# Kernel tuning notes

Hardware: AMD Instinct MI355X
Metric: run time of the kernel (lower is better)

Reference implementation:

```python
import jax, jax.numpy as jnp
import numpy as np

N_NODES = 50000
N_EDGES = 800000
NUM_FEATURES = 256
HIDDEN = 128
NUM_CLASSES = 64


def gcn_conv(x, edge_index, W, b):
    """PyG-style GCNConv: out = D^-1/2 (A+I) D^-1/2 (x W) + b.

    edge_index[0] = source (j), edge_index[1] = target (i);
    messages flow source -> target and are summed at the target.
    """
    n = x.shape[0]
    loop = jnp.arange(n, dtype=edge_index.dtype)
    src = jnp.concatenate([edge_index[0], loop])  # [E+N]
    dst = jnp.concatenate([edge_index[1], loop])  # [E+N]

    h = x @ W  # [N, out_dim] — transform before propagate, as in PyG GCNConv

    deg = jax.ops.segment_sum(jnp.ones_like(dst, dtype=h.dtype), dst, num_segments=n)
    dinv = jnp.where(deg > 0, jax.lax.rsqrt(deg), 0.0)
    norm = dinv[src] * dinv[dst]  # [E+N]

    out = jax.ops.segment_sum(norm[:, None] * h[src], dst, num_segments=n)
    return out + b


def setup_inputs() -> dict:
    key = jax.random.key(0)
    k1, k2, k3, k4 = jax.random.split(key, 4)
    x = jax.random.normal(k1, (N_NODES, NUM_FEATURES), dtype=jnp.float32)
    edge_index = jax.random.randint(k2, (2, N_EDGES), 0, N_NODES, dtype=jnp.int64)
    # Glorot-style init for the two GCN layer weights, zero bias (PyG default)
    W1 = jax.random.normal(k3, (NUM_FEATURES, HIDDEN), dtype=jnp.float32) * (1.0 / np.sqrt(NUM_FEATURES))
    b1 = jnp.zeros((HIDDEN,), dtype=jnp.float32)
    W2 = jax.random.normal(k4, (HIDDEN, NUM_CLASSES), dtype=jnp.float32) * (1.0 / np.sqrt(HIDDEN))
    b2 = jnp.zeros((NUM_CLASSES,), dtype=jnp.float32)
    return {"x": x, "edge_index": edge_index, "W1": W1, "b1": b1, "W2": W2, "b2": b2}


def reference(x, edge_index, W1, b1, W2, b2):
    h = gcn_conv(x, edge_index, W1, b1)
    h = jax.nn.relu(h)
    # dropout(p=0.5, training=True): fixed key stands in for torch RNG
    keep = jax.random.bernoulli(jax.random.key(42), 0.5, h.shape)
    h = jnp.where(keep, h * 2.0, 0.0)
    out = gcn_conv(h, edge_index, W2, b2)
    return out
```

## Files before the change

kernel.cpp:

```cpp
#include <hip/hip_runtime.h>


typedef __attribute__((ext_vector_type(8))) short bf16x8;
typedef __attribute__((ext_vector_type(4))) float f32x4;
typedef __attribute__((ext_vector_type(8))) unsigned short us8;

__device__ __forceinline__ unsigned tf_rotl(unsigned x, int d) {
    return (x << d) | (x >> (32 - d));
}

__device__ __forceinline__ bool dropout_keep(unsigned flat_idx) {
    const unsigned K0 = 0u, K1 = 42u;
    const unsigned K2 = K0 ^ K1 ^ 0x1BD11BDAu;
    unsigned x0 = 0u, x1 = flat_idx;
    x0 += K0; x1 += K1;
#define TF_R(r) { x0 += x1; x1 = tf_rotl(x1, (r)); x1 ^= x0; }
    TF_R(13) TF_R(15) TF_R(26) TF_R(6)
    x0 += K1; x1 += K2 + 1u;
    TF_R(17) TF_R(29) TF_R(16) TF_R(24)
    x0 += K2; x1 += K0 + 2u;
    TF_R(13) TF_R(15) TF_R(26) TF_R(6)
    x0 += K0; x1 += K1 + 3u;
    TF_R(17) TF_R(29) TF_R(16) TF_R(24)
    x0 += K1; x1 += K2 + 4u;
    TF_R(13) TF_R(15) TF_R(26) TF_R(6)
    x0 += K2; x1 += K0 + 5u;
#undef TF_R
    return (((x0 ^ x1) >> 31) & 1u) == 0u;
}

__device__ __forceinline__ unsigned short bf16_rn(float x) {
    unsigned u = __float_as_uint(x);
    unsigned r = u + 0x7FFFu + ((u >> 16) & 1u);
    return (unsigned short)(r >> 16);
}
__device__ __forceinline__ void split_bf16(float x, unsigned short& h, unsigned short& l) {
    h = bf16_rn(x);
    float fh = __uint_as_float(((unsigned)h) << 16);
    l = bf16_rn(x - fh);
}
__device__ __forceinline__ void split4(float4 v, ushort4& h, ushort4& l) {
    unsigned short h0, h1, h2, h3, l0, l1, l2, l3;
    split_bf16(v.x, h0, l0); split_bf16(v.y, h1, l1);
    split_bf16(v.z, h2, l2); split_bf16(v.w, h3, l3);
    h = make_ushort4(h0, h1, h2, h3);
    l = make_ushort4(l0, l1, l2, l3);
}

__device__ __forceinline__ int ei_stride(const int* __restrict__ ei) {
    bool i64 = true;
#pragma unroll
    for (int k = 1; k <= 15; k += 2) i64 = i64 && (ei[k] == 0);
    return i64 ? 2 : 1;
}

template <int K_, int NOUT_, bool SPLITA>
__device__ __forceinline__ void gemm_core(const void* __restrict__ Xv,
                                          const unsigned short* __restrict__ wT_hi,
                                          const unsigned short* __restrict__ wT_lo,
                                          unsigned short* __restrict__ Yb,
                                          int nrows, int bid) {
    constexpr int BM = 64, BK = 32, NKT = K_ / BK;
    constexpr int CT = NOUT_ / 64;
    constexpr int LDW = BK + 8;
    constexpr int WPT = NOUT_ / 32;

    __shared__ __attribute__((aligned(16))) unsigned short xs_hi[BM][LDW];
    __shared__ __attribute__((aligned(16))) unsigned short xs_lo[SPLITA ? BM : 1][SPLITA ? LDW : 1];
    __shared__ __attribute__((aligned(16))) unsigned short ws_hi[NOUT_][LDW];
    __shared__ __attribute__((aligned(16))) unsigned short ws_lo[NOUT_][LDW];

    const int t = threadIdx.x;
    const int wave = t >> 6, lane = t & 63;
    const int m16 = lane & 15, kg = lane >> 4;
    const int row0 = bid * BM;
    const int n0 = wave * (16 * CT);

    const float* Xf = (const float*)Xv;
    const unsigned short* Xb = (const unsigned short*)Xv;

    f32x4 acc[4][CT];
#pragma unroll
    for (int r = 0; r < 4; ++r)
#pragma unroll
        for (int c = 0; c < CT; ++c) acc[r][c] = {0.f, 0.f, 0.f, 0.f};

    float4 xpre[2];
    us8 xpre_b;
    ushort4 wpre_h[WPT], wpre_l[WPT];

    if constexpr (SPLITA) {
#pragma unroll
        for (int i = 0; i < 2; ++i) {
            int idx = t + i * 256;
            int r = idx >> 3, c4 = idx & 7;
            int gr = row0 + r;
            xpre[i] = (gr < nrows) ? *(const float4*)&Xf[(size_t)gr * K_ + c4 * 4]
                                   : make_float4(0.f, 0.f, 0.f, 0.f);
        }
    } else {
        int r = t >> 2, c8 = t & 3;
        int gr = row0 + r;
        xpre_b = (gr < nrows) ? *(const us8*)&Xb[(size_t)gr * K_ + c8 * 8] : (us8)0;
    }
#pragma unroll
    for (int i = 0; i < WPT; ++i) {
        int idx = t + i * 256;
        int n = idx >> 3, c4 = idx & 7;
        wpre_h[i] = *(const ushort4*)&wT_hi[(size_t)n * K_ + c4 * 4];
        wpre_l[i] = *(const ushort4*)&wT_lo[(size_t)n * K_ + c4 * 4];
    }

    for (int kb = 0; kb < NKT; ++kb) {
        if constexpr (SPLITA) {
#pragma unroll
            for (int i = 0; i < 2; ++i) {
                int idx = t + i * 256;
                int r = idx >> 3, c4 = idx & 7;
                ushort4 h, l;
                split4(xpre[i], h, l);
                *(ushort4*)&xs_hi[r][c4 * 4] = h;
                *(ushort4*)&xs_lo[r][c4 * 4] = l;
            }
        } else {
            int r = t >> 2, c8 = t & 3;
            *(us8*)&xs_hi[r][c8 * 8] = xpre_b;
        }
#pragma unroll
        for (int i = 0; i < WPT; ++i) {
            int idx = t + i * 256;
            int n = idx >> 3, c4 = idx & 7;
            *(ushort4*)&ws_hi[n][c4 * 4] = wpre_h[i];
            *(ushort4*)&ws_lo[n][c4 * 4] = wpre_l[i];
        }
        __syncthreads();

        if (kb + 1 < NKT) {
            const int koff = (kb + 1) * BK;
            if constexpr (SPLITA) {
#pragma unroll
                for (int i = 0; i < 2; ++i) {
                    int idx = t + i * 256;
                    int r = idx >> 3, c4 = idx & 7;
                    int gr = row0 + r;
                    xpre[i] = (gr < nrows) ? *(const float4*)&Xf[(size_t)gr * K_ + koff + c4 * 4]
                                           : make_float4(0.f, 0.f, 0.f, 0.f);
                }
            } else {
                int r = t >> 2, c8 = t & 3;
                int gr = row0 + r;
                xpre_b = (gr < nrows) ? *(const us8*)&Xb[(size_t)gr * K_ + koff + c8 * 8] : (us8)0;
            }
#pragma unroll
            for (int i = 0; i < WPT; ++i) {
                int idx = t + i * 256;
                int n = idx >> 3, c4 = idx & 7;
                wpre_h[i] = *(const ushort4*)&wT_hi[(size_t)n * K_ + koff + c4 * 4];
                wpre_l[i] = *(const ushort4*)&wT_lo[(size_t)n * K_ + koff + c4 * 4];
            }
        }

        bf16x8 bh[CT], bl[CT];
#pragma unroll
        for (int c = 0; c < CT; ++c) {
            bh[c] = *(const bf16x8*)&ws_hi[n0 + c * 16 + m16][kg * 8];
            bl[c] = *(const bf16x8*)&ws_lo[n0 + c * 16 + m16][kg * 8];
        }
#pragma unroll
        for (int r = 0; r < 4; ++r) {
            bf16x8 ah = *(const bf16x8*)&xs_hi[r * 16 + m16][kg * 8];
            if constexpr (SPLITA) {
                bf16x8 al = *(const bf16x8*)&xs_lo[r * 16 + m16][kg * 8];
#pragma unroll
                for (int c = 0; c < CT; ++c) {
                    acc[r][c] = __builtin_amdgcn_mfma_f32_16x16x32_bf16(ah, bh[c], acc[r][c], 0, 0, 0);
                    acc[r][c] = __builtin_amdgcn_mfma_f32_16x16x32_bf16(ah, bl[c], acc[r][c], 0, 0, 0);
                    acc[r][c] = __builtin_amdgcn_mfma_f32_16x16x32_bf16(al, bh[c], acc[r][c], 0, 0, 0);
                }
            } else {
#pragma unroll
                for (int c = 0; c < CT; ++c) {
                    acc[r][c] = __builtin_amdgcn_mfma_f32_16x16x32_bf16(ah, bh[c], acc[r][c], 0, 0, 0);
                    acc[r][c] = __builtin_amdgcn_mfma_f32_16x16x32_bf16(ah, bl[c], acc[r][c], 0, 0, 0);
                }
            }
        }
        __syncthreads();
    }

#pragma unroll
    for (int r = 0; r < 4; ++r) {
#pragma unroll
        for (int j = 0; j < 4; ++j) {
            int gr = row0 + r * 16 + kg * 4 + j;
            if (gr < nrows) {
#pragma unroll
                for (int c = 0; c < CT; ++c)
                    Yb[(size_t)gr * NOUT_ + n0 + c * 16 + m16] = bf16_rn(acc[r][c][j]);
            }
        }
    }
}

__global__ __launch_bounds__(256)
void prep(const float* __restrict__ W1, const float* __restrict__ W2,
          unsigned short* __restrict__ wT1_hi, unsigned short* __restrict__ wT1_lo,
          unsigned short* __restrict__ wT2_hi, unsigned short* __restrict__ wT2_lo,
          unsigned* __restrict__ deg, int N) {
    const int b = blockIdx.x, t = threadIdx.x;
    if (b < 160) {
        int idx = b * 256 + t;
        unsigned short h, l;
        if (idx < 256 * 128) {
            int k = idx / 128, n = idx % 128;
            split_bf16(W1[idx], h, l);
            wT1_hi[(size_t)n * 256 + k] = h;
            wT1_lo[(size_t)n * 256 + k] = l;
        } else if (idx < 256 * 128 + 128 * 64) {
            int j = idx - 256 * 128;
            int k = j / 64, n = j % 64;
            split_bf16(W2[j], h, l);
            wT2_hi[(size_t)n * 128 + k] = h;
            wT2_lo[(size_t)n * 128 + k] = l;
        }
    } else {
        int i = (b - 160) * 256 + t;
        if (i < N) deg[i] = 0;
    }
}

__global__ __launch_bounds__(256)
void mega1(const float* __restrict__ x, const unsigned short* __restrict__ wT1_hi,
           const unsigned short* __restrict__ wT1_lo, unsigned short* __restrict__ buffA,
           const int* __restrict__ ei, unsigned* __restrict__ deg,
           unsigned* __restrict__ aux, int N, int E, int nGemm) {
    if ((int)blockIdx.x < nGemm) {
        gemm_core<256, 128, true>(x, wT1_hi, wT1_lo, buffA, N, blockIdx.x);
        return;
    }
    int e = (blockIdx.x - nGemm) * 256 + threadIdx.x;
    if (e >= E) return;
    size_t st = ei_stride(ei);
    aux[e] = atomicAdd(&deg[ei[((size_t)E + e) * st]], 1u);
}

__global__ __launch_bounds__(256)
void scan_phase1(const unsigned* __restrict__ deg, unsigned* __restrict__ blockSums,
                 float* __restrict__ dinv, int N) {
    const int i = blockIdx.x * 256 + threadIdx.x;
    const int lane = threadIdx.x & 63, wave = threadIdx.x >> 6;
    unsigned v = 0;
    if (i < N) {
        unsigned d = deg[i];
        v = (d + 7u) & ~7u;
        dinv[i] = rsqrtf((float)(d + 1u));
    }
    unsigned s = v;
#pragma unroll
    for (int o = 32; o > 0; o >>= 1) s += __shfl_down(s, o, 64);
    __shared__ unsigned ws[4];
    if (lane == 0) ws[wave] = s;
    __syncthreads();
    if (threadIdx.x == 0)
        blockSums[blockIdx.x] = ws[0] + ws[1] + ws[2] + ws[3];
}

__global__ __launch_bounds__(256)
void scan_phase3b(const unsigned* __restrict__ deg, const unsigned* __restrict__ blockSums,
                  unsigned* __restrict__ rowptr, int2* __restrict__ csr2, int N, int nb) {
    __shared__ unsigned s[256];
    const int t = threadIdx.x;

    unsigned bsv = (t < nb) ? blockSums[t] : 0u;
    s[t] = bsv;
    __syncthreads();
    for (int off = 1; off < 256; off <<= 1) {
        unsigned u = (t >= off) ? s[t - off] : 0u;
        __syncthreads();
        s[t] += u;
        __syncthreads();
    }
    const unsigned off0 = (blockIdx.x == 0) ? 0u : s[blockIdx.x - 1];
    __syncthreads();

    const int i = blockIdx.x * 256 + t;
    unsigned d = 0, v = 0;
    if (i < N) { d = deg[i]; v = (d + 7u) & ~7u; }
    s[t] = v;
    __syncthreads();
    for (int off = 1; off < 256; off <<= 1) {
        unsigned u = (t >= off) ? s[t - off] : 0u;
        __syncthreads();
        s[t] += u;
        __syncthreads();
    }
    const unsigned incl = s[t];
    if (i < N) {
        const unsigned rp = off0 + incl - v;
        rowptr[i] = rp;
        if (i == N - 1) rowptr[N] = off0 + incl;
        for (unsigned u = d; u < v; ++u) csr2[rp + u] = make_int2(0, 0);
    }
}

__global__ void place_edges(const int* __restrict__ ei, const unsigned* __restrict__ rowptr,
                            const unsigned* __restrict__ aux, const float* __restrict__ dinv,
                            int2* __restrict__ csr2, int E) {
    int e = blockIdx.x * blockDim.x + threadIdx.x;
    if (e >= E) return;
    size_t st = ei_stride(ei);
    int s = ei[(size_t)e * st];
    int d = ei[((size_t)E + e) * st];
    int2 c;
    c.x = s;
    c.y = __float_as_int(dinv[s] * dinv[d]);
    csr2[rowptr[d] + aux[e]] = c;
}

__global__ __launch_bounds__(256)
void gemm2_kernel(const unsigned short* __restrict__ Xb, const unsigned short* __restrict__ wT_hi,
                  const unsigned short* __restrict__ wT_lo, unsigned short* __restrict__ Yb,
                  int nrows) {
    gemm_core<128, 64, false>(Xb, wT_hi, wT_lo, Yb, nrows, blockIdx.x);
}

__global__ __launch_bounds__(256)
void gather_drop(const unsigned* __restrict__ hs , const int2* __restrict__ csr2,
                 const unsigned* __restrict__ rowptr, const float* __restrict__ dinv,
                 const float* __restrict__ bias, unsigned* __restrict__ outb ,
                 int N) {
    const int node = blockIdx.x * 4 + (threadIdx.x >> 6);
    if (node >= N) return;
    const int lane = threadIdx.x & 63;
    const unsigned beg = rowptr[node];
    const unsigned end = rowptr[node + 1];
    const float dn = dinv[node];
    const float dn2 = dn * dn;

    unsigned v = hs[(size_t)node * 64 + lane];
    float ax = dn2 * __uint_as_float(v << 16);
    float ay = dn2 * __uint_as_float(v & 0xffff0000u);
    for (unsigned k = beg; k < end; k += 8) {
        int2 c[8];
#pragma unroll
        for (int u = 0; u < 8; ++u) c[u] = csr2[k + u];
        unsigned w8[8];
#pragma unroll
        for (int u = 0; u < 8; ++u) w8[u] = hs[(size_t)c[u].x * 64 + lane];
#pragma unroll
        for (int u = 0; u < 8; ++u) {
            float w = __int_as_float(c[u].y);
            ax = fmaf(w, __uint_as_float(w8[u] << 16), ax);
            ay = fmaf(w, __uint_as_float(w8[u] & 0xffff0000u), ay);
        }
    }
    const int f0 = 2 * lane;
    float o0 = fmaxf(ax + bias[f0], 0.0f);
    float o1 = fmaxf(ay + bias[f0 + 1], 0.0f);
    unsigned base = (unsigned)node * 128u + (unsigned)f0;
    o0 = dropout_keep(base) ? 2.0f * o0 : 0.0f;
    o1 = dropout_keep(base + 1u) ? 2.0f * o1 : 0.0f;
    outb[(size_t)node * 64 + lane] =
        (unsigned)bf16_rn(o0) | ((unsigned)bf16_rn(o1) << 16);
}

__global__ __launch_bounds__(256)
void gather_out(const unsigned short* __restrict__ hs , const int2* __restrict__ csr2,
                const unsigned* __restrict__ rowptr, const float* __restrict__ dinv,
                const float* __restrict__ bias, float* __restrict__ outp, int N) {
    const int node = blockIdx.x * 4 + (threadIdx.x >> 6);
    if (node >= N) return;
    const int lane = threadIdx.x & 63;
    const unsigned beg = rowptr[node];
    const unsigned end = rowptr[node + 1];
    const float dn = dinv[node];

    float acc = dn * dn * __uint_as_float(((unsigned)hs[(size_t)node * 64 + lane]) << 16);
    for (unsigned k = beg; k < end; k += 8) {
        int2 c[8];
#pragma unroll
        for (int u = 0; u < 8; ++u) c[u] = csr2[k + u];
        unsigned short w8[8];
#pragma unroll
        for (int u = 0; u < 8; ++u) w8[u] = hs[(size_t)c[u].x * 64 + lane];
#pragma unroll
        for (int u = 0; u < 8; ++u)
            acc = fmaf(__int_as_float(c[u].y), __uint_as_float(((unsigned)w8[u]) << 16), acc);
    }
    outp[(size_t)node * 64 + lane] = acc + bias[lane];
}

extern "C" void kernel_launch(void* const* d_in, const int* in_sizes, int n_in,
                              void* d_out, int out_size, void* d_ws, size_t ws_size,
                              hipStream_t stream) {
    const float* x  = (const float*)d_in[0];
    const int*   ei = (const int*)d_in[1];
    const float* W1 = (const float*)d_in[2];
    const float* b1 = (const float*)d_in[3];
    const float* W2 = (const float*)d_in[4];
    const float* b2 = (const float*)d_in[5];
    float* out = (float*)d_out;

    const int Fdim = 256, Hdim = 128, Cdim = 64;
    const int N = in_sizes[0] / Fdim;
    const int E = in_sizes[1] / 2;
    const int CSR_CAP = E + 7 * N;
    const int NB = (N + 255) / 256;

    unsigned short* wT1_hi = (unsigned short*)d_ws;
    unsigned short* wT1_lo = wT1_hi + 256 * 128;
    unsigned short* wT2_hi = wT1_lo + 256 * 128;
    unsigned short* wT2_lo = wT2_hi + 128 * 64;
    unsigned short* buffA  = wT2_lo + 128 * 64;
    unsigned short* buffB  = buffA + (size_t)N * Hdim;
    unsigned* deg    = (unsigned*)(buffB + (size_t)N * Hdim);
    float*    dinv   = (float*)(deg + N);
    unsigned* rowptr = (unsigned*)(dinv + N);
    unsigned* blockSums = rowptr + (N + 1);
    unsigned* aux    = blockSums + NB;
    uintptr_t csr_p  = ((uintptr_t)(aux + E) + 15) & ~(uintptr_t)15;
    int2*     csr2   = (int2*)csr_p;

    const int nGemm1 = (N + 63) / 64;
    const int nCount = (E + 255) / 256;

    prep<<<160 + (N + 255) / 256, 256, 0, stream>>>(W1, W2, wT1_hi, wT1_lo, wT2_hi, wT2_lo, deg, N);
    mega1<<<nGemm1 + nCount, 256, 0, stream>>>(x, wT1_hi, wT1_lo, buffA, ei, deg, aux, N, E, nGemm1);
    scan_phase1<<<NB, 256, 0, stream>>>(deg, blockSums, dinv, N);
    scan_phase3b<<<NB, 256, 0, stream>>>(deg, blockSums, rowptr, csr2, N, NB);
    place_edges<<<nCount, 256, 0, stream>>>(ei, rowptr, aux, dinv, csr2, E);

    gather_drop<<<(N + 3) / 4, 256, 0, stream>>>((const unsigned*)buffA, csr2, rowptr, dinv, b1,
                                                 (unsigned*)buffB, N);
    gemm2_kernel<<<(N + 63) / 64, 256, 0, stream>>>(buffB, wT2_hi, wT2_lo, buffA, N);
    gather_out<<<(N + 3) / 4, 256, 0, stream>>>(buffA, csr2, rowptr, dinv, b2, out, N);
}
```

Measured before the change: 247.4 us.

## Store CSR as source indices only and load GEMM weights directly into registers

The CSR no longer stores a precomputed per-edge norm. It holds only 4-byte source indices, padded with a dummy node N whose dinv is zero. The gathers look up dinv[src] per neighbour and apply the destination's dinv once at the end, which halves CSR traffic and drops the dinv reads in place_edges, at the cost of extra scattered dinv loads. The GEMM core also drops the shared-memory staging of weights: each lane loads its bf16 weight fragments from global memory into double-buffered registers, removing LDS writes and reads for the B operand at the cost of more register pressure and redundant global loads across blocks. Padding reads row N of buffA, which is never written, but its contribution is multiplied by zero.

```diff
diff --git a/kernel.cpp b/kernel.cpp
--- a/kernel.cpp
+++ b/kernel.cpp
@@ -63,12 +63,9 @@
     constexpr int BM = 64, BK = 32, NKT = K_ / BK;
     constexpr int CT = NOUT_ / 64;
     constexpr int LDW = BK + 8;
-    constexpr int WPT = NOUT_ / 32;
 
     __shared__ __attribute__((aligned(16))) unsigned short xs_hi[BM][LDW];
     __shared__ __attribute__((aligned(16))) unsigned short xs_lo[SPLITA ? BM : 1][SPLITA ? LDW : 1];
-    __shared__ __attribute__((aligned(16))) unsigned short ws_hi[NOUT_][LDW];
-    __shared__ __attribute__((aligned(16))) unsigned short ws_lo[NOUT_][LDW];
 
     const int t = threadIdx.x;
     const int wave = t >> 6, lane = t & 63;
@@ -87,7 +84,7 @@
 
     float4 xpre[2];
     us8 xpre_b;
-    ushort4 wpre_h[WPT], wpre_l[WPT];
+    bf16x8 bh[2][CT], bl[2][CT];
 
     if constexpr (SPLITA) {
 #pragma unroll
@@ -104,14 +101,15 @@
         xpre_b = (gr < nrows) ? *(const us8*)&Xb[(size_t)gr * K_ + c8 * 8] : (us8)0;
     }
 #pragma unroll
-    for (int i = 0; i < WPT; ++i) {
-        int idx = t + i * 256;
-        int n = idx >> 3, c4 = idx & 7;
-        wpre_h[i] = *(const ushort4*)&wT_hi[(size_t)n * K_ + c4 * 4];
-        wpre_l[i] = *(const ushort4*)&wT_lo[(size_t)n * K_ + c4 * 4];
-    }
-
+    for (int c = 0; c < CT; ++c) {
+        const size_t wrow = (size_t)(n0 + c * 16 + m16) * K_ + kg * 8;
+        bh[0][c] = *(const bf16x8*)&wT_hi[wrow];
+        bl[0][c] = *(const bf16x8*)&wT_lo[wrow];
+    }
+
+#pragma unroll
     for (int kb = 0; kb < NKT; ++kb) {
+        const int cur = kb & 1, nxt = cur ^ 1;
         if constexpr (SPLITA) {
 #pragma unroll
             for (int i = 0; i < 2; ++i) {
@@ -125,13 +123,6 @@
         } else {
             int r = t >> 2, c8 = t & 3;
             *(us8*)&xs_hi[r][c8 * 8] = xpre_b;
-        }
-#pragma unroll
-        for (int i = 0; i < WPT; ++i) {
-            int idx = t + i * 256;
-            int n = idx >> 3, c4 = idx & 7;
-            *(ushort4*)&ws_hi[n][c4 * 4] = wpre_h[i];
-            *(ushort4*)&ws_lo[n][c4 * 4] = wpre_l[i];
         }
         __syncthreads();
 
@@ -152,20 +143,13 @@
                 xpre_b = (gr < nrows) ? *(const us8*)&Xb[(size_t)gr * K_ + koff + c8 * 8] : (us8)0;
             }
 #pragma unroll
-            for (int i = 0; i < WPT; ++i) {
-                int idx = t + i * 256;
-                int n = idx >> 3, c4 = idx & 7;
-                wpre_h[i] = *(const ushort4*)&wT_hi[(size_t)n * K_ + koff + c4 * 4];
-                wpre_l[i] = *(const ushort4*)&wT_lo[(size_t)n * K_ + koff + c4 * 4];
+            for (int c = 0; c < CT; ++c) {
+                const size_t wrow = (size_t)(n0 + c * 16 + m16) * K_ + koff + kg * 8;
+                bh[nxt][c] = *(const bf16x8*)&wT_hi[wrow];
+                bl[nxt][c] = *(const bf16x8*)&wT_lo[wrow];
             }
         }
 
-        bf16x8 bh[CT], bl[CT];
-#pragma unroll
-        for (int c = 0; c < CT; ++c) {
-            bh[c] = *(const bf16x8*)&ws_hi[n0 + c * 16 + m16][kg * 8];
-            bl[c] = *(const bf16x8*)&ws_lo[n0 + c * 16 + m16][kg * 8];
-        }
 #pragma unroll
         for (int r = 0; r < 4; ++r) {
             bf16x8 ah = *(const bf16x8*)&xs_hi[r * 16 + m16][kg * 8];
@@ -173,15 +157,15 @@
                 bf16x8 al = *(const bf16x8*)&xs_lo[r * 16 + m16][kg * 8];
 #pragma unroll
                 for (int c = 0; c < CT; ++c) {
-                    acc[r][c] = __builtin_amdgcn_mfma_f32_16x16x32_bf16(ah, bh[c], acc[r][c], 0, 0, 0);
-                    acc[r][c] = __builtin_amdgcn_mfma_f32_16x16x32_bf16(ah, bl[c], acc[r][c], 0, 0, 0);
-                    acc[r][c] = __builtin_amdgcn_mfma_f32_16x16x32_bf16(al, bh[c], acc[r][c], 0, 0, 0);
+                    acc[r][c] = __builtin_amdgcn_mfma_f32_16x16x32_bf16(ah, bh[cur][c], acc[r][c], 0, 0, 0);
+                    acc[r][c] = __builtin_amdgcn_mfma_f32_16x16x32_bf16(ah, bl[cur][c], acc[r][c], 0, 0, 0);
+                    acc[r][c] = __builtin_amdgcn_mfma_f32_16x16x32_bf16(al, bh[cur][c], acc[r][c], 0, 0, 0);
                 }
             } else {
 #pragma unroll
                 for (int c = 0; c < CT; ++c) {
-                    acc[r][c] = __builtin_amdgcn_mfma_f32_16x16x32_bf16(ah, bh[c], acc[r][c], 0, 0, 0);
-                    acc[r][c] = __builtin_amdgcn_mfma_f32_16x16x32_bf16(ah, bl[c], acc[r][c], 0, 0, 0);
+                    acc[r][c] = __builtin_amdgcn_mfma_f32_16x16x32_bf16(ah, bh[cur][c], acc[r][c], 0, 0, 0);
+                    acc[r][c] = __builtin_amdgcn_mfma_f32_16x16x32_bf16(ah, bl[cur][c], acc[r][c], 0, 0, 0);
                 }
             }
         }
@@ -249,6 +233,7 @@
                  float* __restrict__ dinv, int N) {
     const int i = blockIdx.x * 256 + threadIdx.x;
     const int lane = threadIdx.x & 63, wave = threadIdx.x >> 6;
+    if (blockIdx.x == 0 && threadIdx.x == 0) dinv[N] = 0.0f;
     unsigned v = 0;
     if (i < N) {
         unsigned d = deg[i];
@@ -267,7 +252,7 @@
 
 __global__ __launch_bounds__(256)
 void scan_phase3b(const unsigned* __restrict__ deg, const unsigned* __restrict__ blockSums,
-                  unsigned* __restrict__ rowptr, int2* __restrict__ csr2, int N, int nb) {
+                  unsigned* __restrict__ rowptr, int* __restrict__ csr, int N, int nb) {
     __shared__ unsigned s[256];
     const int t = threadIdx.x;
 
@@ -299,22 +284,18 @@
         const unsigned rp = off0 + incl - v;
         rowptr[i] = rp;
         if (i == N - 1) rowptr[N] = off0 + incl;
-        for (unsigned u = d; u < v; ++u) csr2[rp + u] = make_int2(0, 0);
+        for (unsigned u = d; u < v; ++u) csr[rp + u] = N;
     }
 }
 
 __global__ void place_edges(const int* __restrict__ ei, const unsigned* __restrict__ rowptr,
-                            const unsigned* __restrict__ aux, const float* __restrict__ dinv,
-                            int2* __restrict__ csr2, int E) {
+                            const unsigned* __restrict__ aux, int* __restrict__ csr, int E) {
     int e = blockIdx.x * blockDim.x + threadIdx.x;
     if (e >= E) return;
     size_t st = ei_stride(ei);
     int s = ei[(size_t)e * st];
     int d = ei[((size_t)E + e) * st];
-    int2 c;
-    c.x = s;
-    c.y = __float_as_int(dinv[s] * dinv[d]);
-    csr2[rowptr[d] + aux[e]] = c;
+    csr[rowptr[d] + aux[e]] = s;
 }
 
 __global__ __launch_bounds__(256)
@@ -325,7 +306,7 @@
 }
 
 __global__ __launch_bounds__(256)
-void gather_drop(const unsigned* __restrict__ hs , const int2* __restrict__ csr2,
+void gather_drop(const unsigned* __restrict__ hs , const int* __restrict__ csr,
                  const unsigned* __restrict__ rowptr, const float* __restrict__ dinv,
                  const float* __restrict__ bias, unsigned* __restrict__ outb ,
                  int N) {
@@ -335,28 +316,27 @@
     const unsigned beg = rowptr[node];
     const unsigned end = rowptr[node + 1];
     const float dn = dinv[node];
-    const float dn2 = dn * dn;
 
     unsigned v = hs[(size_t)node * 64 + lane];
-    float ax = dn2 * __uint_as_float(v << 16);
-    float ay = dn2 * __uint_as_float(v & 0xffff0000u);
+    float ax = dn * __uint_as_float(v << 16);
+    float ay = dn * __uint_as_float(v & 0xffff0000u);
     for (unsigned k = beg; k < end; k += 8) {
-        int2 c[8];
-#pragma unroll
-        for (int u = 0; u < 8; ++u) c[u] = csr2[k + u];
+        int j[8];
+#pragma unroll
+        for (int u = 0; u < 8; ++u) j[u] = csr[k + u];
         unsigned w8[8];
-#pragma unroll
-        for (int u = 0; u < 8; ++u) w8[u] = hs[(size_t)c[u].x * 64 + lane];
+        float dv[8];
+#pragma unroll
+        for (int u = 0; u < 8; ++u) { w8[u] = hs[(size_t)j[u] * 64 + lane]; dv[u] = dinv[j[u]]; }
 #pragma unroll
         for (int u = 0; u < 8; ++u) {
-            float w = __int_as_float(c[u].y);
-            ax = fmaf(w, __uint_as_float(w8[u] << 16), ax);
-            ay = fmaf(w, __uint_as_float(w8[u] & 0xffff0000u), ay);
+            ax = fmaf(dv[u], __uint_as_float(w8[u] << 16), ax);
+            ay = fmaf(dv[u], __uint_as_float(w8[u] & 0xffff0000u), ay);
         }
     }
     const int f0 = 2 * lane;
-    float o0 = fmaxf(ax + bias[f0], 0.0f);
-    float o1 = fmaxf(ay + bias[f0 + 1], 0.0f);
+    float o0 = fmaxf(fmaf(dn, ax, bias[f0]), 0.0f);
+    float o1 = fmaxf(fmaf(dn, ay, bias[f0 + 1]), 0.0f);
     unsigned base = (unsigned)node * 128u + (unsigned)f0;
     o0 = dropout_keep(base) ? 2.0f * o0 : 0.0f;
     o1 = dropout_keep(base + 1u) ? 2.0f * o1 : 0.0f;
@@ -365,7 +345,7 @@
 }
 
 __global__ __launch_bounds__(256)
-void gather_out(const unsigned short* __restrict__ hs , const int2* __restrict__ csr2,
+void gather_out(const unsigned short* __restrict__ hs , const int* __restrict__ csr,
                 const unsigned* __restrict__ rowptr, const float* __restrict__ dinv,
                 const float* __restrict__ bias, float* __restrict__ outp, int N) {
     const int node = blockIdx.x * 4 + (threadIdx.x >> 6);
@@ -375,19 +355,20 @@
     const unsigned end = rowptr[node + 1];
     const float dn = dinv[node];
 
-    float acc = dn * dn * __uint_as_float(((unsigned)hs[(size_t)node * 64 + lane]) << 16);
+    float acc = dn * __uint_as_float(((unsigned)hs[(size_t)node * 64 + lane]) << 16);
     for (unsigned k = beg; k < end; k += 8) {
-        int2 c[8];
-#pragma unroll
-        for (int u = 0; u < 8; ++u) c[u] = csr2[k + u];
+        int j[8];
+#pragma unroll
+        for (int u = 0; u < 8; ++u) j[u] = csr[k + u];
         unsigned short w8[8];
-#pragma unroll
-        for (int u = 0; u < 8; ++u) w8[u] = hs[(size_t)c[u].x * 64 + lane];
+        float dv[8];
+#pragma unroll
+        for (int u = 0; u < 8; ++u) { w8[u] = hs[(size_t)j[u] * 64 + lane]; dv[u] = dinv[j[u]]; }
 #pragma unroll
         for (int u = 0; u < 8; ++u)
-            acc = fmaf(__int_as_float(c[u].y), __uint_as_float(((unsigned)w8[u]) << 16), acc);
-    }
-    outp[(size_t)node * 64 + lane] = acc + bias[lane];
+            acc = fmaf(dv[u], __uint_as_float(((unsigned)w8[u]) << 16), acc);
+    }
+    outp[(size_t)node * 64 + lane] = fmaf(dn, acc, bias[lane]);
 }
 
 extern "C" void kernel_launch(void* const* d_in, const int* in_sizes, int n_in,
@@ -412,26 +393,25 @@
     unsigned short* wT2_hi = wT1_lo + 256 * 128;
     unsigned short* wT2_lo = wT2_hi + 128 * 64;
     unsigned short* buffA  = wT2_lo + 128 * 64;
-    unsigned short* buffB  = buffA + (size_t)N * Hdim;
+    unsigned short* buffB  = buffA + (size_t)(N + 1) * Hdim;
     unsigned* deg    = (unsigned*)(buffB + (size_t)N * Hdim);
     float*    dinv   = (float*)(deg + N);
-    unsigned* rowptr = (unsigned*)(dinv + N);
+    unsigned* rowptr = (unsigned*)(dinv + (N + 1));
     unsigned* blockSums = rowptr + (N + 1);
     unsigned* aux    = blockSums + NB;
-    uintptr_t csr_p  = ((uintptr_t)(aux + E) + 15) & ~(uintptr_t)15;
-    int2*     csr2   = (int2*)csr_p;
+    int*      csr    = (int*)(aux + E);
 
     const int nGemm1 = (N + 63) / 64;
     const int nCount = (E + 255) / 256;
 
-    prep<<<160 + (N + 255) / 256, 256, 0, stream>>>(W1, W2, wT1_hi, wT1_lo, wT2_hi, wT2_lo, deg, N);
+    prep<<<160 + NB, 256, 0, stream>>>(W1, W2, wT1_hi, wT1_lo, wT2_hi, wT2_lo, deg, N);
     mega1<<<nGemm1 + nCount, 256, 0, stream>>>(x, wT1_hi, wT1_lo, buffA, ei, deg, aux, N, E, nGemm1);
     scan_phase1<<<NB, 256, 0, stream>>>(deg, blockSums, dinv, N);
-    scan_phase3b<<<NB, 256, 0, stream>>>(deg, blockSums, rowptr, csr2, N, NB);
-    place_edges<<<nCount, 256, 0, stream>>>(ei, rowptr, aux, dinv, csr2, E);
-
-    gather_drop<<<(N + 3) / 4, 256, 0, stream>>>((const unsigned*)buffA, csr2, rowptr, dinv, b1,
+    scan_phase3b<<<NB, 256, 0, stream>>>(deg, blockSums, rowptr, csr, N, NB);
+    place_edges<<<nCount, 256, 0, stream>>>(ei, rowptr, aux, csr, E);
+
+    gather_drop<<<(N + 3) / 4, 256, 0, stream>>>((const unsigned*)buffA, csr, rowptr, dinv, b1,
                                                  (unsigned*)buffB, N);
     gemm2_kernel<<<(N + 63) / 64, 256, 0, stream>>>(buffB, wT2_hi, wT2_lo, buffA, N);
-    gather_out<<<(N + 3) / 4, 256, 0, stream>>>(buffA, csr2, rowptr, dinv, b2, out, N);
-}
+    gather_out<<<(N + 3) / 4, 256, 0, stream>>>(buffA, csr, rowptr, dinv, b2, out, N);
+}
```

New measurement: 232.9 us. -5.8%, faster.
